# Performance work log

Measured on AMD Instinct MI355X. Metric: run time of the kernel, lower is better.

The kernel has to match this reference:

```python
import jax, jax.numpy as jnp
import numpy as np

B, L, C, H, W = 2, 8, 64, 128, 128
HID = 256


def setup_inputs() -> dict:
    key = jax.random.key(0)
    k0, k1, k2, k3, k4 = jax.random.split(key, 5)
    x = jax.random.normal(k0, (B, L, C, H, W), dtype=jnp.float32)
    # Conv2d(in*4 -> hidden, kernel=1): weight stored as [out, in] for 1x1
    conv_w = jax.random.normal(k1, (HID, 4 * C), dtype=jnp.float32) * (1.0 / np.sqrt(4 * C))
    conv_b = jax.random.normal(k2, (HID,), dtype=jnp.float32) * 0.01
    conv_out_w = jax.random.normal(k3, (4 * C, HID), dtype=jnp.float32) * (1.0 / np.sqrt(HID))
    conv_out_b = jax.random.normal(k4, (4 * C,), dtype=jnp.float32) * 0.01
    return {"x": x, "conv_w": conv_w, "conv_b": conv_b,
            "conv_out_w": conv_out_w, "conv_out_b": conv_out_b}


def _dwt(x):  # x: [N, C, Hp, Wp] (even dims) -> [N, 4C, Hp/2, Wp/2]
    x1 = x[:, :, 0::2, 0::2] * 0.5
    x2 = x[:, :, 1::2, 0::2] * 0.5
    x3 = x[:, :, 0::2, 1::2] * 0.5
    x4 = x[:, :, 1::2, 1::2] * 0.5
    return jnp.concatenate([x1 + x2 + x3 + x4,
                            -x1 - x2 + x3 + x4,
                            -x1 + x2 - x3 + x4,
                            x1 - x2 - x3 + x4], axis=1)


def _idwt(y):  # y: [N, 4C, Hh, Wh] -> [N, C, 2Hh, 2Wh]
    n, c4, hh, wh = y.shape
    co = c4 // 4
    y1 = y[:, 0 * co:1 * co] * 0.5
    y2 = y[:, 1 * co:2 * co] * 0.5
    y3 = y[:, 2 * co:3 * co] * 0.5
    y4 = y[:, 3 * co:4 * co] * 0.5
    a = y1 - y2 - y3 + y4   # h[0::2, 0::2]
    b = y1 - y2 + y3 - y4   # h[1::2, 0::2]
    c = y1 + y2 - y3 - y4   # h[0::2, 1::2]
    d = y1 + y2 + y3 + y4   # h[1::2, 1::2]
    r0 = jnp.stack([a, c], axis=-1).reshape(n, co, hh, 2 * wh)  # even rows
    r1 = jnp.stack([b, d], axis=-1).reshape(n, co, hh, 2 * wh)  # odd rows
    return jnp.stack([r0, r1], axis=-2).reshape(n, co, 2 * hh, 2 * wh)


def reference(x, conv_w, conv_b, conv_out_w, conv_out_b):
    b, l, c, h, w = x.shape
    pad_h = (2 - h % 2) % 2
    pad_w = (2 - w % 2) % 2
    if pad_h > 0 or pad_w > 0:
        x = jnp.pad(x, ((0, 0), (0, 0), (0, 0), (0, pad_h), (0, pad_w)))
    hp, wp = x.shape[-2], x.shape[-1]
    xf = x.reshape(b * l, c, hp, wp)
    x_dwt = _dwt(xf)                                       # [BL, 4C, hp/2, wp/2]
    feat = jnp.einsum('nchw,oc->nohw', x_dwt, conv_w) + conv_b[None, :, None, None]
    feat = jax.nn.silu(feat)
    y = jnp.einsum('nchw,oc->nohw', feat, conv_out_w) + conv_out_b[None, :, None, None]
    rec = _idwt(y)                                         # [BL, C, hp, wp]
    out = rec.reshape(b, l, c, hp, wp)
    if pad_h > 0 or pad_w > 0:
        out = out[..., :h, :w]
    return out
```

## Files before the change

kernel.cpp:

```cpp
#include <hip/hip_runtime.h>
#include <hip/hip_bf16.h>


typedef __bf16 bf16x8 __attribute__((ext_vector_type(8)));
typedef float  f32x4  __attribute__((ext_vector_type(4)));

#define SP 264

__device__ __forceinline__ unsigned short f2bf(float f) {
  __hip_bfloat16 h = __float2bfloat16(f);
  return __builtin_bit_cast(unsigned short, h);
}
__device__ __forceinline__ float bf2f(unsigned short s) {
  union { unsigned int i; float f; } v; v.i = ((unsigned int)s) << 16; return v.f;
}
__device__ __forceinline__ float silu(float f) {
  return f / (1.0f + __expf(-f));
}
__device__ __forceinline__ bf16x8 ldw8(const float* __restrict__ p) {
  const float4 a = *(const float4*)p;
  const float4 b = *(const float4*)(p + 4);
  bf16x8 r;
  r[0] = (__bf16)a.x; r[1] = (__bf16)a.y; r[2] = (__bf16)a.z; r[3] = (__bf16)a.w;
  r[4] = (__bf16)b.x; r[5] = (__bf16)b.y; r[6] = (__bf16)b.z; r[7] = (__bf16)b.w;
  return r;
}

__global__ __launch_bounds__(256) void cvt_w(const float* __restrict__ w1,
                                             const float* __restrict__ w2,
                                             unsigned short* __restrict__ o) {
  const int i = (blockIdx.x * 256 + threadIdx.x) * 4;
  const float4 a = *(const float4*)(w1 + i);
  const float4 b = *(const float4*)(w2 + i);
  *(ushort4*)(o + i)         = make_ushort4(f2bf(a.x), f2bf(a.y), f2bf(a.z), f2bf(a.w));
  *(ushort4*)(o + 65536 + i) = make_ushort4(f2bf(b.x), f2bf(b.y), f2bf(b.z), f2bf(b.w));
}

template <bool WBF16>
__global__ __launch_bounds__(256, 4)
void wavelet_fused(const float* __restrict__ x,
                   const void* __restrict__ w1p,
                   const float* __restrict__ b1,
                   const void* __restrict__ w2p,
                   const float* __restrict__ b2,
                   float* __restrict__ out)
{
  __shared__ unsigned short lds[64 * SP];

  const int t  = threadIdx.x;
  const int n  = blockIdx.x >> 6;
  const int hh = blockIdx.x & 63;

  const int ww = t & 63;
  const int cg = t >> 6;

  {
    const float* xb = x + ((size_t)n * 64 * 128 + (size_t)(2 * hh)) * 128 + 2 * ww;
    #pragma unroll
    for (int j = 0; j < 4; ++j) {
      const int c0 = (cg + 4 * j) * 4;
      float qv[4][4];
      #pragma unroll
      for (int ci = 0; ci < 4; ++ci) {
        const float* p = xb + (size_t)(c0 + ci) * (128 * 128);
        const float2 r0 = *(const float2*)p;
        const float2 r1 = *(const float2*)(p + 128);
        const float x1 = r0.x, x3 = r0.y;
        const float x2 = r1.x, x4 = r1.y;
        qv[0][ci] = 0.5f * ((x1 + x2) + (x3 + x4));
        qv[1][ci] = 0.5f * ((x3 + x4) - (x1 + x2));
        qv[2][ci] = 0.5f * ((x2 + x4) - (x1 + x3));
        qv[3][ci] = 0.5f * ((x1 + x4) - (x2 + x3));
      }
      #pragma unroll
      for (int q = 0; q < 4; ++q) {
        ushort4 v = make_ushort4(f2bf(qv[q][0]), f2bf(qv[q][1]), f2bf(qv[q][2]), f2bf(qv[q][3]));
        *(ushort4*)(&lds[ww * SP + q * 64 + c0]) = v;
      }
    }
  }
  __syncthreads();

  const int wv   = t >> 6;
  const int r    = t & 15;
  const int quad = (t & 63) >> 4;

  {
    f32x4 acc[4][4];
    #pragma unroll
    for (int mt = 0; mt < 4; ++mt)
      #pragma unroll
      for (int nt = 0; nt < 4; ++nt)
        acc[mt][nt] = (f32x4){0.0f, 0.0f, 0.0f, 0.0f};

    #pragma unroll
    for (int k0 = 0; k0 < 256; k0 += 32) {
      bf16x8 a[4], b[4];
      #pragma unroll
      for (int mt = 0; mt < 4; ++mt) {
        const int row = wv * 64 + mt * 16 + r;
        if constexpr (WBF16)
          a[mt] = *(const bf16x8*)((const unsigned short*)w1p + row * 256 + quad * 8 + k0);
        else
          a[mt] = ldw8((const float*)w1p + row * 256 + quad * 8 + k0);
      }
      #pragma unroll
      for (int nt = 0; nt < 4; ++nt)
        b[nt] = *(const bf16x8*)(&lds[(nt * 16 + r) * SP + quad * 8 + k0]);
      #pragma unroll
      for (int mt = 0; mt < 4; ++mt)
        #pragma unroll
        for (int nt = 0; nt < 4; ++nt)
          acc[mt][nt] = __builtin_amdgcn_mfma_f32_16x16x32_bf16(a[mt], b[nt], acc[mt][nt], 0, 0, 0);
    }
    __syncthreads();

    #pragma unroll
    for (int mt = 0; mt < 4; ++mt) {
      const int ob = wv * 64 + mt * 16 + quad * 4;
      const float4 bb = *(const float4*)(b1 + ob);
      #pragma unroll
      for (int nt = 0; nt < 4; ++nt) {
        const int pix = nt * 16 + r;
        ushort4 v;
        v.x = f2bf(silu(acc[mt][nt][0] + bb.x));
        v.y = f2bf(silu(acc[mt][nt][1] + bb.y));
        v.z = f2bf(silu(acc[mt][nt][2] + bb.z));
        v.w = f2bf(silu(acc[mt][nt][3] + bb.w));
        *(ushort4*)(&lds[pix * SP + ob]) = v;
      }
    }
  }
  __syncthreads();

  {
    f32x4 acc[4][4];
    #pragma unroll
    for (int mt = 0; mt < 4; ++mt)
      #pragma unroll
      for (int nt = 0; nt < 4; ++nt)
        acc[mt][nt] = (f32x4){0.0f, 0.0f, 0.0f, 0.0f};

    #pragma unroll
    for (int k0 = 0; k0 < 256; k0 += 32) {
      bf16x8 a[4], b[4];
      #pragma unroll
      for (int mt = 0; mt < 4; ++mt) {
        const int row = wv * 64 + mt * 16 + r;
        if constexpr (WBF16)
          a[mt] = *(const bf16x8*)((const unsigned short*)w2p + row * 256 + quad * 8 + k0);
        else
          a[mt] = ldw8((const float*)w2p + row * 256 + quad * 8 + k0);
      }
      #pragma unroll
      for (int nt = 0; nt < 4; ++nt)
        b[nt] = *(const bf16x8*)(&lds[(nt * 16 + r) * SP + quad * 8 + k0]);
      #pragma unroll
      for (int mt = 0; mt < 4; ++mt)
        #pragma unroll
        for (int nt = 0; nt < 4; ++nt)
          acc[mt][nt] = __builtin_amdgcn_mfma_f32_16x16x32_bf16(a[mt], b[nt], acc[mt][nt], 0, 0, 0);
    }
    __syncthreads();

    #pragma unroll
    for (int mt = 0; mt < 4; ++mt) {
      const int cb = wv * 64 + mt * 16 + quad * 4;
      const float4 bb = *(const float4*)(b2 + cb);
      #pragma unroll
      for (int nt = 0; nt < 4; ++nt) {
        const int pix = nt * 16 + r;
        ushort4 v;
        v.x = f2bf(acc[mt][nt][0] + bb.x);
        v.y = f2bf(acc[mt][nt][1] + bb.y);
        v.z = f2bf(acc[mt][nt][2] + bb.z);
        v.w = f2bf(acc[mt][nt][3] + bb.w);
        *(ushort4*)(&lds[pix * SP + cb]) = v;
      }
    }
  }
  __syncthreads();

  {
    float* ob_ = out + ((size_t)n * 64 * 128 + (size_t)(2 * hh)) * 128 + 2 * ww;
    #pragma unroll
    for (int j = 0; j < 4; ++j) {
      const int c0 = (cg + 4 * j) * 4;
      unsigned short yb[4][4];
      #pragma unroll
      for (int q = 0; q < 4; ++q) {
        const ushort4 v = *(const ushort4*)(&lds[ww * SP + q * 64 + c0]);
        yb[q][0] = v.x; yb[q][1] = v.y; yb[q][2] = v.z; yb[q][3] = v.w;
      }
      #pragma unroll
      for (int ci = 0; ci < 4; ++ci) {
        const float y1 = 0.5f * bf2f(yb[0][ci]);
        const float y2 = 0.5f * bf2f(yb[1][ci]);
        const float y3 = 0.5f * bf2f(yb[2][ci]);
        const float y4 = 0.5f * bf2f(yb[3][ci]);
        const float s14 = y1 + y4, s23 = y2 + y3;
        const float d14 = y1 - y4, d23 = y2 - y3;
        const float oa  = s14 - s23;
        const float oc  = d14 + d23;
        const float obv = d14 - d23;
        const float od  = s14 + s23;
        float* prow = ob_ + (size_t)(c0 + ci) * (128 * 128);
        *(float2*)prow         = make_float2(oa, oc);
        *(float2*)(prow + 128) = make_float2(obv, od);
      }
    }
  }
}

extern "C" void kernel_launch(void* const* d_in, const int* in_sizes, int n_in,
                              void* d_out, int out_size, void* d_ws, size_t ws_size,
                              hipStream_t stream) {
  (void)in_sizes; (void)n_in; (void)out_size;
  const float* x  = (const float*)d_in[0];
  const float* w1 = (const float*)d_in[1];
  const float* b1 = (const float*)d_in[2];
  const float* w2 = (const float*)d_in[3];
  const float* b2 = (const float*)d_in[4];
  float* o = (float*)d_out;

  if (ws_size >= 2u * 65536u * sizeof(unsigned short)) {
    unsigned short* wb = (unsigned short*)d_ws;
    cvt_w<<<dim3(64), dim3(256), 0, stream>>>(w1, w2, wb);
    wavelet_fused<true><<<dim3(16 * 64), dim3(256), 0, stream>>>(
        x, wb, b1, wb + 65536, b2, o);
  } else {
    wavelet_fused<false><<<dim3(16 * 64), dim3(256), 0, stream>>>(
        x, w1, b1, w2, b2, o);
  }
}
```

Before: 155.1 us.

## Process two rows per block, prefetching second row's input during first GEMMs

Result: faster. 147.8 us (-4.7%).

```diff
diff --git a/kernel.cpp b/kernel.cpp
--- a/kernel.cpp
+++ b/kernel.cpp
@@ -36,51 +36,54 @@
   *(ushort4*)(o + 65536 + i) = make_ushort4(f2bf(b.x), f2bf(b.y), f2bf(b.z), f2bf(b.w));
 }
 
+__device__ __forceinline__ void load_st(const float* __restrict__ x, int n, int hh,
+                                        int ww, int cg, float2 (&st)[32]) {
+  const float* xb = x + ((size_t)n * 64 * 128 + (size_t)(2 * hh)) * 128 + 2 * ww;
+  #pragma unroll
+  for (int j = 0; j < 4; ++j) {
+    const int c0 = (cg + 4 * j) * 4;
+    #pragma unroll
+    for (int ci = 0; ci < 4; ++ci) {
+      const float* p = xb + (size_t)(c0 + ci) * (128 * 128);
+      st[(j * 4 + ci) * 2]     = *(const float2*)p;
+      st[(j * 4 + ci) * 2 + 1] = *(const float2*)(p + 128);
+    }
+  }
+}
+
+__device__ __forceinline__ void dwt_write(const float2 (&st)[32], unsigned short* lds,
+                                          int ww, int cg) {
+  #pragma unroll
+  for (int j = 0; j < 4; ++j) {
+    const int c0 = (cg + 4 * j) * 4;
+    float qv[4][4];
+    #pragma unroll
+    for (int ci = 0; ci < 4; ++ci) {
+      const float2 r0 = st[(j * 4 + ci) * 2];
+      const float2 r1 = st[(j * 4 + ci) * 2 + 1];
+      const float x1 = r0.x, x3 = r0.y;
+      const float x2 = r1.x, x4 = r1.y;
+      qv[0][ci] = 0.5f * ((x1 + x2) + (x3 + x4));
+      qv[1][ci] = 0.5f * ((x3 + x4) - (x1 + x2));
+      qv[2][ci] = 0.5f * ((x2 + x4) - (x1 + x3));
+      qv[3][ci] = 0.5f * ((x1 + x4) - (x2 + x3));
+    }
+    #pragma unroll
+    for (int q = 0; q < 4; ++q) {
+      ushort4 v = make_ushort4(f2bf(qv[q][0]), f2bf(qv[q][1]), f2bf(qv[q][2]), f2bf(qv[q][3]));
+      *(ushort4*)(&lds[ww * SP + q * 64 + c0]) = v;
+    }
+  }
+}
+
 template <bool WBF16>
-__global__ __launch_bounds__(256, 4)
-void wavelet_fused(const float* __restrict__ x,
-                   const void* __restrict__ w1p,
-                   const float* __restrict__ b1,
-                   const void* __restrict__ w2p,
-                   const float* __restrict__ b2,
-                   float* __restrict__ out)
-{
-  __shared__ unsigned short lds[64 * SP];
-
-  const int t  = threadIdx.x;
-  const int n  = blockIdx.x >> 6;
-  const int hh = blockIdx.x & 63;
-
-  const int ww = t & 63;
-  const int cg = t >> 6;
-
-  {
-    const float* xb = x + ((size_t)n * 64 * 128 + (size_t)(2 * hh)) * 128 + 2 * ww;
-    #pragma unroll
-    for (int j = 0; j < 4; ++j) {
-      const int c0 = (cg + 4 * j) * 4;
-      float qv[4][4];
-      #pragma unroll
-      for (int ci = 0; ci < 4; ++ci) {
-        const float* p = xb + (size_t)(c0 + ci) * (128 * 128);
-        const float2 r0 = *(const float2*)p;
-        const float2 r1 = *(const float2*)(p + 128);
-        const float x1 = r0.x, x3 = r0.y;
-        const float x2 = r1.x, x4 = r1.y;
-        qv[0][ci] = 0.5f * ((x1 + x2) + (x3 + x4));
-        qv[1][ci] = 0.5f * ((x3 + x4) - (x1 + x2));
-        qv[2][ci] = 0.5f * ((x2 + x4) - (x1 + x3));
-        qv[3][ci] = 0.5f * ((x1 + x4) - (x2 + x3));
-      }
-      #pragma unroll
-      for (int q = 0; q < 4; ++q) {
-        ushort4 v = make_ushort4(f2bf(qv[q][0]), f2bf(qv[q][1]), f2bf(qv[q][2]), f2bf(qv[q][3]));
-        *(ushort4*)(&lds[ww * SP + q * 64 + c0]) = v;
-      }
-    }
-  }
-  __syncthreads();
-
+__device__ __forceinline__ void process_row(unsigned short* lds,
+                                            const void* __restrict__ w1p,
+                                            const float* __restrict__ b1,
+                                            const void* __restrict__ w2p,
+                                            const float* __restrict__ b2,
+                                            float* __restrict__ out, int n, int hh,
+                                            int t, int ww, int cg) {
   const int wv   = t >> 6;
   const int r    = t & 15;
   const int quad = (t & 63) >> 4;
@@ -212,6 +215,43 @@
   }
 }
 
+template <bool WBF16>
+__global__ __launch_bounds__(256, 2)
+void wavelet_fused(const float* __restrict__ x,
+                   const void* __restrict__ w1p,
+                   const float* __restrict__ b1,
+                   const void* __restrict__ w2p,
+                   const float* __restrict__ b2,
+                   float* __restrict__ out)
+{
+  __shared__ unsigned short lds[64 * SP];
+
+  const int t  = threadIdx.x;
+  const int ww = t & 63;
+  const int cg = t >> 6;
+
+  const int idx0 = blockIdx.x;
+  const int idx1 = blockIdx.x + 512;
+  const int n0 = idx0 >> 6, hh0 = idx0 & 63;
+  const int n1 = idx1 >> 6, hh1 = idx1 & 63;
+
+  float2 st[32];
+
+  load_st(x, n0, hh0, ww, cg, st);
+  dwt_write(st, lds, ww, cg);
+  __syncthreads();
+
+  load_st(x, n1, hh1, ww, cg, st);
+
+  process_row<WBF16>(lds, w1p, b1, w2p, b2, out, n0, hh0, t, ww, cg);
+
+  __syncthreads();
+  dwt_write(st, lds, ww, cg);
+  __syncthreads();
+
+  process_row<WBF16>(lds, w1p, b1, w2p, b2, out, n1, hh1, t, ww, cg);
+}
+
 extern "C" void kernel_launch(void* const* d_in, const int* in_sizes, int n_in,
                               void* d_out, int out_size, void* d_ws, size_t ws_size,
                               hipStream_t stream) {
@@ -226,10 +266,10 @@
   if (ws_size >= 2u * 65536u * sizeof(unsigned short)) {
     unsigned short* wb = (unsigned short*)d_ws;
     cvt_w<<<dim3(64), dim3(256), 0, stream>>>(w1, w2, wb);
-    wavelet_fused<true><<<dim3(16 * 64), dim3(256), 0, stream>>>(
+    wavelet_fused<true><<<dim3(512), dim3(256), 0, stream>>>(
         x, wb, b1, wb + 65536, b2, o);
   } else {
-    wavelet_fused<false><<<dim3(16 * 64), dim3(256), 0, stream>>>(
+    wavelet_fused<false><<<dim3(512), dim3(256), 0, stream>>>(
         x, w1, b1, w2, b2, o);
   }
 }
```
